# Performance work log

Hardware: AMD Instinct MI355X
Metric: run time of the kernel (lower is better)

## Reference

```python
import jax, jax.numpy as jnp
import numpy as np

CH = 192; NH = 8; HD = CH // NH; WS = 8; OV = 2; WSO = WS + 2 * OV
SCALE = HD ** -0.5
B, H, W = 2, 256, 256

# static relative-position index (matches WindowMSA._idx)
_gy, _gx = np.meshgrid(np.arange(WS), np.arange(WS), indexing='ij')
_flat = np.stack([_gy.ravel(), _gx.ravel()])            # [2, ws*ws]
_rel = _flat[:, :, None] - _flat[:, None, :]
_rel[0] += WS - 1; _rel[1] += WS - 1; _rel[0] *= 2 * WS - 1
RPE_IDX = jnp.asarray(_rel.sum(0), dtype=jnp.int32)     # [64, 64]


def _ln(x, g, b, eps=1e-5):
    m = jnp.mean(x, -1, keepdims=True)
    v = jnp.mean((x - m) ** 2, -1, keepdims=True)
    return (x - m) * jax.lax.rsqrt(v + eps) * g + b


def _partition(xhw):  # [B,H,W,C] -> [B*nw, ws*ws, C]
    b, h, w, c = xhw.shape
    x = xhw.reshape(b, h // WS, WS, w // WS, WS, c).transpose(0, 1, 3, 2, 4, 5)
    return x.reshape(-1, WS * WS, c)


def _reverse(xw, h, w, b):  # [B*nw, ws*ws, C] -> [B,H,W,C]
    c = xw.shape[-1]
    x = xw.reshape(b, h // WS, w // WS, WS, WS, c).transpose(0, 1, 3, 2, 4, 5)
    return x.reshape(b, h, w, c)


def _mha(q, k, v, bias=None):  # q:[n,Nq,C] k,v:[n,Nk,C] split into heads
    n, nq, c = q.shape
    nk = k.shape[1]
    q = q.reshape(n, nq, NH, HD).transpose(0, 2, 1, 3)
    k = k.reshape(n, nk, NH, HD).transpose(0, 2, 1, 3)
    v = v.reshape(n, nk, NH, HD).transpose(0, 2, 1, 3)
    attn = jnp.einsum('bhnd,bhmd->bhnm', q, k) * SCALE
    if bias is not None:
        attn = attn + bias
    attn = jax.nn.softmax(attn, axis=-1)
    out = jnp.einsum('bhnm,bhmd->bhnd', attn, v)
    return out.transpose(0, 2, 1, 3).reshape(n, nq, c)


def _forward(x, g1, b1, qkv_w, rpe, wproj_w, g2, b2, mlp_w1, mlp_w2,
             alpha, og, ob, q_w, kv_w, oproj_w):
    b, c, h, w = x.shape  # H,W are multiples of WS -> no window padding
    xhw = x.transpose(0, 2, 3, 1)  # BHWC

    # --- window MSA branch (shift=False) ---
    xw = _partition(xhw)  # [b*nw, 64, C]
    xn = _ln(xw, g1, b1)
    qkv = xn @ qkv_w.T  # [n, 64, 3C]
    q, k, v = jnp.split(qkv, 3, axis=-1)
    bias = rpe[RPE_IDX].transpose(2, 0, 1)[None]  # [1, nh, 64, 64]
    msa = _mha(q, k, v, bias) @ wproj_w.T
    xw = xw + msa
    hmid = _ln(xw, g2, b2) @ mlp_w1.T
    xw = xw + jax.nn.gelu(hmid, approximate=False) @ mlp_w2.T
    x_win = _reverse(xw, h, w, b).transpose(0, 3, 1, 2)  # BCHW

    # --- overlapping cross attention branch ---
    xwin = _partition(xhw)  # queries from non-overlapped windows [n, 64, C]
    q = _ln(xwin, og, ob) @ q_w.T
    xp2 = jnp.pad(x, ((0, 0), (0, 0), (OV, OV), (OV, OV)), mode='reflect')
    xp2 = xp2.transpose(0, 2, 3, 1)  # [B, H+2ov, W+2ov, C]
    nh_w, nw_w = h // WS, w // WS
    rows = (jnp.arange(nh_w) * WS)[:, None] + jnp.arange(WSO)[None, :]
    cols = (jnp.arange(nw_w) * WS)[:, None] + jnp.arange(WSO)[None, :]
    xuf = xp2[:, rows]            # [B, nh_w, wso, W+2ov, C]
    xuf = xuf[:, :, :, cols]      # [B, nh_w, wso, nw_w, wso, C]
    xuf = xuf.transpose(0, 1, 3, 2, 4, 5).reshape(-1, WSO * WSO, c)
    kv = xuf @ kv_w.T             # [n, 144, 2C]
    k, v = jnp.split(kv, 2, axis=-1)
    out = _mha(q, k, v) @ oproj_w.T + xwin
    x_oca = _reverse(out, h, w, b).transpose(0, 3, 1, 2)

    return x + x_win * alpha + x_oca * (1.0 - alpha)


def setup_inputs():
    key = jax.random.key(0)
    ks = jax.random.split(key, 10)
    f = lambda k, shape: jax.random.normal(k, shape, jnp.float32) * 0.02
    return {
        'x': jax.random.normal(ks[0], (B, CH, H, W), jnp.float32),
        'g1': jnp.ones((CH,), jnp.float32), 'b1': jnp.zeros((CH,), jnp.float32),
        'qkv_w': f(ks[1], (3 * CH, CH)),
        'rpe': f(ks[2], ((2 * WS - 1) ** 2, NH)),
        'wproj_w': f(ks[3], (CH, CH)),
        'g2': jnp.ones((CH,), jnp.float32), 'b2': jnp.zeros((CH,), jnp.float32),
        'mlp_w1': f(ks[4], (2 * CH, CH)), 'mlp_w2': f(ks[5], (CH, 2 * CH)),
        'alpha': jnp.float32(0.5),
        'og': jnp.ones((CH,), jnp.float32), 'ob': jnp.zeros((CH,), jnp.float32),
        'q_w': f(ks[6], (CH, CH)), 'kv_w': f(ks[7], (2 * CH, CH)),
        'oproj_w': f(ks[8], (CH, CH)),
    }


def reference(x, g1, b1, qkv_w, rpe, wproj_w, g2, b2, mlp_w1, mlp_w2,
              alpha, og, ob, q_w, kv_w, oproj_w):
    return _forward(x, g1, b1, qkv_w, rpe, wproj_w, g2, b2, mlp_w1, mlp_w2,
                    alpha, og, ob, q_w, kv_w, oproj_w)
```

## Files before the change

kernel.cpp:

```cpp
#include <hip/hip_runtime.h>
#include <hip/hip_bf16.h>

typedef unsigned short u16;
typedef unsigned int   u32;
typedef __attribute__((ext_vector_type(8))) short bf16x8;
typedef __attribute__((ext_vector_type(4))) float f32x4;

#define CH   192
#define NH   8
#define HWD  256
#define LDW  200
#define QSTR 28
#define SCALE 0.20412414523193154f

__device__ __forceinline__ float bf2f(u16 u){ u32 v = ((u32)u) << 16; return __builtin_bit_cast(float, v); }
__device__ __forceinline__ u16 f2bf(float f){
  u32 u = __builtin_bit_cast(u32, f);
  u = (u + 0x7fffu + ((u >> 16) & 1u)) >> 16;
  return (u16)u;
}
__device__ __forceinline__ float lo2f(u32 p){ return __builtin_bit_cast(float, p << 16); }
__device__ __forceinline__ float hi2f(u32 p){ return __builtin_bit_cast(float, p & 0xffff0000u); }
__device__ __forceinline__ void up8(uint4 q, float* f){
  f[0]=lo2f(q.x); f[1]=hi2f(q.x); f[2]=lo2f(q.y); f[3]=hi2f(q.y);
// ... 311 lines not shown
      for (int j = 0; j < 6; ++j)
        acc[j] = mfma16(a, bfrag(WO, (half*6 + j)*6 + kt, l), acc[j]);
    }
    __syncthreads();
    #pragma unroll
    for (int j = 0; j < 6; ++j){
      int col = (half*6 + j)*16 + (l & 15);
      #pragma unroll
      for (int r = 0; r < 4; ++r)
        pool[XO_ + (rbase + r)*LDW + col] = f2bf(acc[j][r]);
    }
  }
  __syncthreads();

  if (MODE == 0){
    float beta = 1.f - alpha_p[0];
    float xg = 1.f + beta;
    for (int j = tid; j < 1536; j += 512){
      int c = j >> 3, ty = j & 7;
      size_t goff = ((size_t)c*HWD + hrow + ty)*HWD + wcol;
      const float* src = xb + goff;
      float4 a = *reinterpret_cast<const float4*>(src);
      float4 q = *reinterpret_cast<const float4*>(src + 4);
      float wv[8];
      #pragma unroll
      for (int e = 0; e < 8; ++e) wv[e] = bf2f(pool[XO_ + (ty*8 + e)*LDW + c]);
      float4 o1 = make_float4(xg*a.x + beta*wv[0], xg*a.y + beta*wv[1], xg*a.z + beta*wv[2], xg*a.w + beta*wv[3]);
      float4 o2 = make_float4(xg*q.x + beta*wv[4], xg*q.y + beta*wv[5], xg*q.z + beta*wv[6], xg*q.w + beta*wv[7]);
      *reinterpret_cast<float4*>(outb + goff)     = o1;
      *reinterpret_cast<float4*>(outb + goff + 4) = o2;
    }
  } else {
    u16* xw = xoca + (size_t)win*12288;
    for (int j = tid; j < 1536; j += 512){
      int c = j >> 3, ty = j & 7;
      size_t goff = ((size_t)c*HWD + hrow + ty)*HWD + wcol;
      const float* src = xb + goff;
      float4 a = *reinterpret_cast<const float4*>(src);
      float4 q = *reinterpret_cast<const float4*>(src + 4);
      float xv[8] = {a.x,a.y,a.z,a.w,q.x,q.y,q.z,q.w};
      u32 wds[4];
      #pragma unroll
      for (int e = 0; e < 4; ++e){
        u32 lo = f2bf(bf2f(pool[XO_ + (ty*8 + 2*e  )*LDW + c]) + xv[2*e]);
        u32 hi = f2bf(bf2f(pool[XO_ + (ty*8 + 2*e+1)*LDW + c]) + xv[2*e+1]);
        wds[e] = lo | (hi << 16);
      }
      uint4 o; o.x = wds[0]; o.y = wds[1]; o.z = wds[2]; o.w = wds[3];
      *reinterpret_cast<uint4*>(xw + c*64 + ty*8) = o;
    }
  }
}

#define MSX  0
#define MSQ  12800
#define MKF  25600
#define MVT  41984
#define MP0  60416
#define MP1  65024
#define MSN  25600
#define MXW  38400
#define MSG  0
#define MSTM 69632
#define MSTS 70656
#define MST  71168
#define MPOOL 71424

template<int MODE>
__global__ __launch_bounds__(512) void k_msa(
    const float* __restrict__ x, const u16* __restrict__ ws16, const float* __restrict__ wsf,
    const float* __restrict__ rpe, const float* __restrict__ alpha_p, float* __restrict__ out,
    const u16* __restrict__ xoca)
{
  __shared__ __align__(16) u16 pool[MPOOL];
  float* stm = reinterpret_cast<float*>(pool + MSTM);
  float* sts = reinterpret_cast<float*>(pool + MSTS);
  float* st  = reinterpret_cast<float*>(pool + MST);
  const u16* W1  = ws16 + WS_W1/2;
  const u16* WP  = ws16 + WS_WP/2;
  const u16* WM1 = ws16 + WS_WM1/2;
  const u16* WM2 = ws16 + WS_WM2/2;
  const float* c1  = wsf + WS_C1/4;
  const float* c2  = wsf + WS_C2/4;
  const float* c1m = wsf + WS_C1M/4;
  const float* c2m = wsf + WS_C2M/4;

  const int tid = threadIdx.x;
  const int win = blockIdx.x;
  const int b  = win >> 10;
  const int wy = (win >> 5) & 31;
  const int wx = win & 31;
  const int hrow = wy*8, wcol = wx*8;
  const float* xb = x + (size_t)b*CH*HWD*HWD;
  float* outb = out + (size_t)b*CH*HWD*HWD;
  const f32x4 z4 = {0.f,0.f,0.f,0.f};

  for (int j = tid; j < 1536; j += 512){
    int c = j >> 3, ty = j & 7;
    const float* src = xb + ((size_t)c*HWD + hrow + ty)*HWD + wcol;
    float4 a = *reinterpret_cast<const float4*>(src);
    float4 q = *reinterpret_cast<const float4*>(src + 4);
    u16* dst = &pool[MSX + (ty*8)*LDW + c];
    dst[0*LDW]=f2bf(a.x); dst[1*LDW]=f2bf(a.y); dst[2*LDW]=f2bf(a.z); dst[3*LDW]=f2bf(a.w);
    dst[4*LDW]=f2bf(q.x); dst[5*LDW]=f2bf(q.y); dst[6*LDW]=f2bf(q.z); dst[7*LDW]=f2bf(q.w);
  }
  {
    const uint4 zz = make_uint4(0,0,0,0);
    for (int i = tid; i < 2048; i += 512)
      *reinterpret_cast<uint4*>(pool + MKF + i*8) = zz;
    for (int i = tid; i < 2304; i += 512)
      *reinterpret_cast<uint4*>(pool + MVT + i*8) = zz;
    for (int i = tid; i < 64; i += 512)
      *reinterpret_cast<uint4*>(pool + MSQ + i*LDW + 192) = zz;
  }
  __syncthreads();
  ln_stats(pool + MSX, st, tid);
  __syncthreads();

  const int w = tid >> 6, l = tid & 63;
  const int mt = w >> 1, half = w & 1;
  const int arow = mt*16 + (l & 15);
  const int rbase = mt*16 + ((l>>4)<<2);

  {
    f32x4 acc[18];
    #pragma unroll
    for (int j = 0; j < 18; ++j) acc[j] = z4;
    for (int kt = 0; kt < 6; ++kt){
      bf16x8 a = afrag(pool, MSX, LDW, arow, kt, l);
      #pragma unroll
      for (int j = 0; j < 18; ++j)
        acc[j] = mfma16(a, bfrag(W1, (half*18 + j)*6 + kt, l), acc[j]);
    }
    float mr[4], rr[4];
    #pragma unroll
    for (int r = 0; r < 4; ++r){ mr[r] = st[(rbase+r)*2]; rr[r] = st[(rbase+r)*2+1]; }
    #pragma unroll
    for (int j = 0; j < 18; ++j){
      int tile = half*18 + j;
      int col = tile*16 + (l & 15);
      float c1v = c1[col], c2v = c2[col];
      if (tile < 12){
        #pragma unroll
        for (int r = 0; r < 4; ++r){
          int row = rbase + r;
          float v = rr[r]*(acc[j][r] - mr[r]*c1v) + c2v;
          pool[MSQ + row*LDW + col] = f2bf(SCALE*v);
        }
      } else if (tile < 24){
        int d = col - 192; int h = d/24; int dd = d - h*24;
        int base = MKF + h*2048 + ((((dd>>3)<<4))<<3) + (dd&7);
        #pragma unroll
        for (int r = 0; r < 4; ++r){
          int row = rbase + r;
          float v = rr[r]*(acc[j][r] - mr[r]*c1v) + c2v;
          pool[base + ((row>>4)<<9) + ((row&15)<<3)] = f2bf(v);
        }
      } else {
        int d = col - 384; int h = d/24; int dd = d - h*24;
        int base = MVT + h*2304 + dd*72;
        #pragma unroll
        for (int r = 0; r < 4; ++r){
          int row = rbase + r;
          float v = rr[r]*(acc[j][r] - mr[r]*c1v) + c2v;
          pool[base + row] = f2bf(v);
        }
      }
    }
  }
  __syncthreads();

  {
    const int ng = half;
    int bidx[2][4];
    #pragma unroll
    for (int t = 0; t < 2; ++t)
      #pragma unroll
      for (int r = 0; r < 4; ++r){
        int row = rbase + r, col = (ng*2 + t)*16 + (l & 15);
        bidx[t][r] = (((row>>3)-(col>>3)+7)*15 + ((row&7)-(col&7)+7))*NH;
      }
    for (int hg = 0; hg < 2; ++hg){
      f32x4 S[4][2];
      #pragma unroll
      for (int hh = 0; hh < 4; ++hh){
        int h = hg*4 + hh;
        bf16x8 a = *reinterpret_cast<const bf16x8*>(pool + MSQ + arow*LDW + h*24 + ((l>>4)<<3));
        #pragma unroll
        for (int t = 0; t < 2; ++t)
          S[hh][t] = mfma16(a, *reinterpret_cast<const bf16x8*>(pool + MKF + h*2048 + (ng*2+t)*512 + l*8), z4);
      }
      #pragma unroll
      for (int hh = 0; hh < 4; ++hh){
        int h = hg*4 + hh;
        #pragma unroll
        for (int t = 0; t < 2; ++t)
          #pragma unroll
          for (int r = 0; r < 4; ++r)
            S[hh][t][r] += rpe[bidx[t][r] + h];
        #pragma unroll
        for (int r = 0; r < 4; ++r){
          float mx = fmaxf(S[hh][0][r], S[hh][1][r]);
          mx = fmaxf(mx, __shfl_xor(mx, 1, 64));
          mx = fmaxf(mx, __shfl_xor(mx, 2, 64));
          mx = fmaxf(mx, __shfl_xor(mx, 4, 64));
          mx = fmaxf(mx, __shfl_xor(mx, 8, 64));
          if ((l & 15) == 0) stm[hh*128 + (rbase+r)*2 + ng] = mx;
        }
      }
      __syncthreads();
      #pragma unroll
      for (int hh = 0; hh < 4; ++hh){
        int h = hg*4 + hh;
        u16* Pb = pool + ((h & 1) ? MP1 : MP0);
        float* sb = sts + (h & 1)*128;
        #pragma unroll
        for (int r = 0; r < 4; ++r){
          int row = rbase + r;
          float m = fmaxf(stm[hh*128 + row*2], stm[hh*128 + row*2 + 1]);
          float sum = 0.f;
          #pragma unroll
          for (int t = 0; t < 2; ++t){
            float p = __expf(S[hh][t][r] - m);
            sum += p;
            Pb[row*72 + (ng*2+t)*16 + (l & 15)] = f2bf(p);
          }
          sum += __shfl_xor(sum, 1, 64);
          sum += __shfl_xor(sum, 2, 64);
          sum += __shfl_xor(sum, 4, 64);
          sum += __shfl_xor(sum, 8, 64);
          if ((l & 15) == 0) sb[row*2 + ng] = sum;
        }
        __syncthreads();
        f32x4 O = z4;
        #pragma unroll
        for (int kt = 0; kt < 2; ++kt){
          bf16x8 pa = *reinterpret_cast<const bf16x8*>(Pb + arow*72 + kt*32 + ((l>>4)<<3));
          bf16x8 vb = *reinterpret_cast<const bf16x8*>(pool + MVT + h*2304 + (ng*16 + (l & 15))*72 + kt*32 + ((l>>4)<<3));
          O = mfma16(pa, vb, O);
        }
        int d = ng*16 + (l & 15);
        if (d < 24){
          #pragma unroll
          for (int r = 0; r < 4; ++r){
            int row = rbase + r;
            float inv = 1.f / (sb[row*2] + sb[row*2 + 1]);
            pool[MSQ + row*LDW + h*24 + d] = f2bf(O[r]*inv);
          }
        }
      }
    }
  }
  __syncthreads();

  {
    f32x4 acc[6];
    #pragma unroll
    for (int j = 0; j < 6; ++j) acc[j] = z4;
    for (int kt = 0; kt < 6; ++kt){
      bf16x8 a = afrag(pool, MSQ, LDW, arow, kt, l);
      #pragma unroll
      for (int j = 0; j < 6; ++j)
        acc[j] = mfma16(a, bfrag(WP, (half*6 + j)*6 + kt, l), acc[j]);
    }
    __syncthreads();
    #pragma unroll
    for (int j = 0; j < 6; ++j){
      int col = (half*6 + j)*16 + (l & 15);
      #pragma unroll
      for (int r = 0; r < 4; ++r){
        int row = rbase + r;
        pool[MSN + row*LDW + col] = f2bf(acc[j][r] + bf2f(pool[MSX + row*LDW + col]));
      }
    }
  }
  __syncthreads();
  ln_stats(pool + MSN, st, tid);
  __syncthreads();

  {
    f32x4 acc[12];
    #pragma unroll
    for (int j = 0; j < 12; ++j) acc[j] = z4;
    for (int kt = 0; kt < 6; ++kt){
      bf16x8 a = afrag(pool, MSN, LDW, arow, kt, l);
      #pragma unroll
      for (int j = 0; j < 12; ++j)
        acc[j] = mfma16(a, bfrag(WM1, (half*12 + j)*6 + kt, l), acc[j]);
    }
    float mr[4], rr[4];
    #pragma unroll
    for (int r = 0; r < 4; ++r){ mr[r] = st[(rbase+r)*2]; rr[r] = st[(rbase+r)*2+1]; }
    __syncthreads();
    #pragma unroll
    for (int j = 0; j < 12; ++j){
      int col = (half*12 + j)*16 + (l & 15);
      float c1v = c1m[col], c2v = c2m[col];
      #pragma unroll
      for (int r = 0; r < 4; ++r){
        float hv = rr[r]*(acc[j][r] - mr[r]*c1v) + c2v;
        float gl = 0.5f*hv*(1.f + erff(hv*0.70710678118654752f));
        pool[MSG + (rbase + r)*392 + col] = f2bf(gl);
      }
    }
  }
  __syncthreads();

  {
    f32x4 acc[6];
    #pragma unroll
    for (int j = 0; j < 6; ++j) acc[j] = z4;
    for (int kt = 0; kt < 12; ++kt){
      bf16x8 a = afrag(pool, MSG, 392, arow, kt, l);
      #pragma unroll
      for (int j = 0; j < 6; ++j)
        acc[j] = mfma16(a, bfrag(WM2, (half*6 + j)*12 + kt, l), acc[j]);
    }
    #pragma unroll
    for (int j = 0; j < 6; ++j){
      int col = (half*6 + j)*16 + (l & 15);
      #pragma unroll
      for (int r = 0; r < 4; ++r){
        int row = rbase + r;
        pool[MXW + row*LDW + col] = f2bf(acc[j][r] + bf2f(pool[MSN + row*LDW + col]));
      }
    }
  }
  __syncthreads();

  float alpha = alpha_p[0];
  if (MODE == 0){
    for (int j = tid; j < 1536; j += 512){
      int c = j >> 3, ty = j & 7;
      size_t goff = ((size_t)c*HWD + hrow + ty)*HWD + wcol;
      float* dst = outb + goff;
      float4 a = *reinterpret_cast<const float4*>(dst);
      float4 q = *reinterpret_cast<const float4*>(dst + 4);
      float wv[8];
      #pragma unroll
      for (int e = 0; e < 8; ++e) wv[e] = bf2f(pool[MXW + (ty*8 + e)*LDW + c]);
      float4 o1 = make_float4(a.x + alpha*wv[0], a.y + alpha*wv[1], a.z + alpha*wv[2], a.w + alpha*wv[3]);
      float4 o2 = make_float4(q.x + alpha*wv[4], q.y + alpha*wv[5], q.z + alpha*wv[6], q.w + alpha*wv[7]);
      *reinterpret_cast<float4*>(dst)     = o1;
      *reinterpret_cast<float4*>(dst + 4) = o2;
    }
  } else {
    float beta = 1.f - alpha;
    const u16* xw = xoca + (size_t)win*12288;
    for (int j = tid; j < 1536; j += 512){
      int c = j >> 3, ty = j & 7;
      size_t goff = ((size_t)c*HWD + hrow + ty)*HWD + wcol;
      const float* src = xb + goff;
      float4 a = *reinterpret_cast<const float4*>(src);
      float4 q = *reinterpret_cast<const float4*>(src + 4);
      uint4 oc = *reinterpret_cast<const uint4*>(xw + c*64 + ty*8);
      float ov[8]; up8(oc, ov);
      float wv[8];
      #pragma unroll
      for (int e = 0; e < 8; ++e) wv[e] = bf2f(pool[MXW + (ty*8 + e)*LDW + c]);
      float4 o1 = make_float4(a.x + alpha*wv[0] + beta*ov[0], a.y + alpha*wv[1] + beta*ov[1],
                              a.z + alpha*wv[2] + beta*ov[2], a.w + alpha*wv[3] + beta*ov[3]);
      float4 o2 = make_float4(q.x + alpha*wv[4] + beta*ov[4], q.y + alpha*wv[5] + beta*ov[5],
                              q.z + alpha*wv[6] + beta*ov[6], q.w + alpha*wv[7] + beta*ov[7]);
      *reinterpret_cast<float4*>(outb + goff)     = o1;
      *reinterpret_cast<float4*>(outb + goff + 4) = o2;
    }
  }
}

__device__ __forceinline__ void layernorm_fb(const u16* __restrict__ src, u16* __restrict__ dst,
                                             const float* __restrict__ g, const float* __restrict__ b,
                                             int tid)
{
  int r = tid >> 3, sub = tid & 7;
  const u16* row = src + r*LDW + sub*24;
  float v[24];
  float s = 0.f, s2 = 0.f;
  #pragma unroll
  for (int e = 0; e < 24; ++e){ v[e] = bf2f(row[e]); s += v[e]; s2 += v[e]*v[e]; }
  s  += __shfl_xor(s, 1, 64);  s  += __shfl_xor(s, 2, 64);  s  += __shfl_xor(s, 4, 64);
  s2 += __shfl_xor(s2, 1, 64); s2 += __shfl_xor(s2, 2, 64); s2 += __shfl_xor(s2, 4, 64);
  float m   = s * (1.f/192.f);
  float var = s2 * (1.f/192.f) - m*m;
  float rs  = rsqrtf(var + 1e-5f);
  u16* drow = dst + r*LDW + sub*24;
  #pragma unroll
  for (int e = 0; e < 24; ++e)
    drow[e] = f2bf((v[e] - m) * rs * g[sub*24+e] + b[sub*24+e]);
}
__device__ __forceinline__ void gemm83(const u16* __restrict__ a_lds,
                                       const float* __restrict__ w0,
                                       const float* __restrict__ w1,
                                       const float* __restrict__ w2,
                                       int tg, float (*acc)[3])
{
  for (int k0 = 0; k0 < 192; k0 += 8){
    float wv[3][8];
    ldw8(w0 + k0, wv[0]); ldw8(w1 + k0, wv[1]); ldw8(w2 + k0, wv[2]);
    #pragma unroll
    for (int tt = 0; tt < 8; ++tt){
      float a[8];
      up8(*reinterpret_cast<const uint4*>(a_lds + (tg*8+tt)*LDW + k0), a);
      #pragma unroll
      for (int e = 0; e < 8; ++e){
        acc[tt][0] += a[e]*wv[0][e];
        acc[tt][1] += a[e]*wv[1][e];
        acc[tt][2] += a[e]*wv[2][e];
      }
    }
  }
}
__global__ __launch_bounds__(512) void k_msa_fb(
// ... 368 lines not shown
```

Baseline: 950.6 us.

## Shrink MSA kernel LDS footprint by staging K/V per head-group

Shared memory for the window MSA kernel is cut from about 140KB to about 75KB. The QKV accumulators now stay in registers, and K/V are scattered into LDS four heads at a time, once per head group. The projection residual is re-read from global x instead of being kept in LDS, and a single P buffer replaces the double-buffered one. The goal is to fit two 512-thread blocks per CU for better latency hiding, at the cost of holding 18 accumulators in registers across the attention loop, extra barriers, and uncoalesced global reads for the residual.

Measured after the change: 1.191 ms, median of 4. 1.25x slower.

```diff
diff --git a/kernel.cpp b/kernel.cpp
--- a/kernel.cpp
+++ b/kernel.cpp
@@ -387,19 +387,18 @@
   }
 }
 
-#define MSX  0
-#define MSQ  12800
-#define MKF  25600
-#define MVT  41984
-#define MP0  60416
-#define MP1  65024
-#define MSN  25600
-#define MXW  38400
-#define MSG  0
-#define MSTM 69632
-#define MSTS 70656
-#define MST  71168
-#define MPOOL 71424
+#define KFGm  0
+#define VTGm  8192
+#define MSXm  0
+#define MSQm  17408
+#define PBUFm 30208
+#define STMm  34816
+#define STSm  35840
+#define MSNm  0
+#define MSGm  12800
+#define MXWm  12800
+#define STLNm 37888
+#define MPOOLm 38144
 
 template<int MODE>
 __global__ __launch_bounds__(512) void k_msa(
@@ -407,10 +406,10 @@
     const float* __restrict__ rpe, const float* __restrict__ alpha_p, float* __restrict__ out,
     const u16* __restrict__ xoca)
 {
-  __shared__ __align__(16) u16 pool[MPOOL];
-  float* stm = reinterpret_cast<float*>(pool + MSTM);
-  float* sts = reinterpret_cast<float*>(pool + MSTS);
-  float* st  = reinterpret_cast<float*>(pool + MST);
+  __shared__ __align__(16) u16 pool[MPOOLm];
+  float* stm = reinterpret_cast<float*>(pool + STMm);
+  float* sts = reinterpret_cast<float*>(pool + STSm);
+  float* st  = reinterpret_cast<float*>(pool + STLNm);
   const u16* W1  = ws16 + WS_W1/2;
   const u16* WP  = ws16 + WS_WP/2;
   const u16* WM1 = ws16 + WS_WM1/2;
@@ -435,229 +434,249 @@
     const float* src = xb + ((size_t)c*HWD + hrow + ty)*HWD + wcol;
     float4 a = *reinterpret_cast<const float4*>(src);
     float4 q = *reinterpret_cast<const float4*>(src + 4);
-    u16* dst = &pool[MSX + (ty*8)*LDW + c];
+    u16* dst = &pool[MSXm + (ty*8)*LDW + c];
     dst[0*LDW]=f2bf(a.x); dst[1*LDW]=f2bf(a.y); dst[2*LDW]=f2bf(a.z); dst[3*LDW]=f2bf(a.w);
     dst[4*LDW]=f2bf(q.x); dst[5*LDW]=f2bf(q.y); dst[6*LDW]=f2bf(q.z); dst[7*LDW]=f2bf(q.w);
   }
   {
     const uint4 zz = make_uint4(0,0,0,0);
-    for (int i = tid; i < 2048; i += 512)
-      *reinterpret_cast<uint4*>(pool + MKF + i*8) = zz;
-    for (int i = tid; i < 2304; i += 512)
-      *reinterpret_cast<uint4*>(pool + MVT + i*8) = zz;
     for (int i = tid; i < 64; i += 512)
-      *reinterpret_cast<uint4*>(pool + MSQ + i*LDW + 192) = zz;
-  }
-  __syncthreads();
-  ln_stats(pool + MSX, st, tid);
+      *reinterpret_cast<uint4*>(pool + MSQm + i*LDW + 192) = zz;
+  }
+  __syncthreads();
+  ln_stats(pool + MSXm, st, tid);
   __syncthreads();
 
   const int w = tid >> 6, l = tid & 63;
   const int mt = w >> 1, half = w & 1;
   const int arow = mt*16 + (l & 15);
   const int rbase = mt*16 + ((l>>4)<<2);
+  const int ng = half;
+
+  f32x4 acc[18];
+  #pragma unroll
+  for (int j = 0; j < 18; ++j) acc[j] = z4;
+  for (int kt = 0; kt < 6; ++kt){
+    bf16x8 a = afrag(pool, MSXm, LDW, arow, kt, l);
+    #pragma unroll
+    for (int j = 0; j < 18; ++j)
+      acc[j] = mfma16(a, bfrag(W1, (half*18 + j)*6 + kt, l), acc[j]);
+  }
+  float mr[4], rr[4];
+  #pragma unroll
+  for (int r = 0; r < 4; ++r){ mr[r] = st[(rbase+r)*2]; rr[r] = st[(rbase+r)*2+1]; }
+  __syncthreads();
+
+  #define SCAT(J, TILE) do{                                                     \
+    int col = (TILE)*16 + (l & 15);                                             \
+    float c1v = c1[col], c2v = c2[col];                                         \
+    if ((TILE) < 12){                                                           \
+      _Pragma("unroll")                                                         \
+      for (int r = 0; r < 4; ++r){                                              \
+        int row = rbase + r;                                                    \
+        float v = rr[r]*(acc[J][r] - mr[r]*c1v) + c2v;                          \
+        pool[MSQm + row*LDW + col] = f2bf(SCALE*v);                             \
+      }                                                                         \
+    } else if ((TILE) < 24){                                                    \
+      int d = col - 192; int h = d/24; int dd = d - h*24;                       \
+      int base = KFGm + (h&3)*2048 + ((dd>>3)<<7) + (dd&7);                     \
+      _Pragma("unroll")                                                         \
+      for (int r = 0; r < 4; ++r){                                              \
+        int row = rbase + r;                                                    \
+        float v = rr[r]*(acc[J][r] - mr[r]*c1v) + c2v;                          \
+        pool[base + ((row>>4)<<9) + ((row&15)<<3)] = f2bf(v);                   \
+      }                                                                         \
+    } else {                                                                    \
+      int d = col - 384; int h = d/24; int dd = d - h*24;                       \
+      int base = VTGm + (h&3)*2304 + dd*72;                                     \
+      _Pragma("unroll")                                                         \
+      for (int r = 0; r < 4; ++r){                                              \
+        int row = rbase + r;                                                    \
+        float v = rr[r]*(acc[J][r] - mr[r]*c1v) + c2v;                          \
+        pool[base + row] = f2bf(v);                                             \
+      }                                                                         \
+    }                                                                           \
+  } while(0)
 
   {
-    f32x4 acc[18];
-    #pragma unroll
-    for (int j = 0; j < 18; ++j) acc[j] = z4;
-    for (int kt = 0; kt < 6; ++kt){
-      bf16x8 a = afrag(pool, MSX, LDW, arow, kt, l);
-      #pragma unroll
-      for (int j = 0; j < 18; ++j)
-        acc[j] = mfma16(a, bfrag(W1, (half*18 + j)*6 + kt, l), acc[j]);
-    }
-    float mr[4], rr[4];
-    #pragma unroll
-    for (int r = 0; r < 4; ++r){ mr[r] = st[(rbase+r)*2]; rr[r] = st[(rbase+r)*2+1]; }
-    #pragma unroll
-    for (int j = 0; j < 18; ++j){
-      int tile = half*18 + j;
-      int col = tile*16 + (l & 15);
-      float c1v = c1[col], c2v = c2[col];
-      if (tile < 12){
+    const uint4 zz = make_uint4(0,0,0,0);
+    for (int i = tid; i < 256; i += 512)
+      *reinterpret_cast<uint4*>(pool + KFGm + (i>>4)*512 + (48 + (i&15))*8) = zz;
+    for (int i = tid; i < 288; i += 512){
+      int slot = i/72; int t2 = i - slot*72; int dd = 24 + t2/9; int seg = t2 - (t2/9)*9;
+      *reinterpret_cast<uint4*>(pool + VTGm + slot*2304 + dd*72 + seg*8) = zz;
+    }
+  }
+
+  int bidx[2][4];
+  #pragma unroll
+  for (int t = 0; t < 2; ++t)
+    #pragma unroll
+    for (int r = 0; r < 4; ++r){
+      int row = rbase + r, col = (ng*2 + t)*16 + (l & 15);
+      bidx[t][r] = (((row>>3)-(col>>3)+7)*15 + ((row&7)-(col&7)+7))*NH;
+    }
+
+  for (int hg = 0; hg < 2; ++hg){
+    if (hg == 0){
+      if (half == 0){
+        #pragma unroll
+        for (int j = 0; j < 18; ++j) SCAT(j, j);
+      } else {
+        #pragma unroll
+        for (int j = 6; j < 12; ++j) SCAT(j, 18 + j);
+      }
+    } else {
+      if (half == 1){
+        #pragma unroll
+        for (int j = 0; j < 6; ++j)  SCAT(j, 18 + j);
+        #pragma unroll
+        for (int j = 12; j < 18; ++j) SCAT(j, 18 + j);
+      }
+    }
+    __syncthreads();
+
+    f32x4 S[4][2];
+    #pragma unroll
+    for (int hh = 0; hh < 4; ++hh){
+      int h = hg*4 + hh;
+      bf16x8 a = *reinterpret_cast<const bf16x8*>(pool + MSQm + arow*LDW + h*24 + ((l>>4)<<3));
+      #pragma unroll
+      for (int t = 0; t < 2; ++t)
+        S[hh][t] = mfma16(a, *reinterpret_cast<const bf16x8*>(pool + KFGm + (h&3)*2048 + (ng*2+t)*512 + l*8), z4);
+    }
+    #pragma unroll
+    for (int hh = 0; hh < 4; ++hh){
+      int h = hg*4 + hh;
+      #pragma unroll
+      for (int t = 0; t < 2; ++t)
+        #pragma unroll
+        for (int r = 0; r < 4; ++r)
+          S[hh][t][r] += rpe[bidx[t][r] + h];
+      #pragma unroll
+      for (int r = 0; r < 4; ++r){
+        float mx = fmaxf(S[hh][0][r], S[hh][1][r]);
+        mx = fmaxf(mx, __shfl_xor(mx, 1, 64));
+        mx = fmaxf(mx, __shfl_xor(mx, 2, 64));
+        mx = fmaxf(mx, __shfl_xor(mx, 4, 64));
+        mx = fmaxf(mx, __shfl_xor(mx, 8, 64));
+        if ((l & 15) == 0) stm[hh*128 + (rbase+r)*2 + ng] = mx;
+      }
+    }
+    __syncthreads();
+
+    #pragma unroll
+    for (int hh = 0; hh < 4; ++hh){
+      int h = hg*4 + hh;
+      #pragma unroll
+      for (int r = 0; r < 4; ++r){
+        int row = rbase + r;
+        float m = fmaxf(stm[hh*128 + row*2], stm[hh*128 + row*2 + 1]);
+        float sum = 0.f;
+        #pragma unroll
+        for (int t = 0; t < 2; ++t){
+          float p = __expf(S[hh][t][r] - m);
+          sum += p;
+          pool[PBUFm + row*72 + (ng*2+t)*16 + (l & 15)] = f2bf(p);
+        }
+        sum += __shfl_xor(sum, 1, 64);
+        sum += __shfl_xor(sum, 2, 64);
+        sum += __shfl_xor(sum, 4, 64);
+        sum += __shfl_xor(sum, 8, 64);
+        if ((l & 15) == 0) sts[row*2 + ng] = sum;
+      }
+      __syncthreads();
+      f32x4 O = z4;
+      #pragma unroll
+      for (int kt = 0; kt < 2; ++kt){
+        bf16x8 pa = *reinterpret_cast<const bf16x8*>(pool + PBUFm + arow*72 + kt*32 + ((l>>4)<<3));
+        bf16x8 vb = *reinterpret_cast<const bf16x8*>(pool + VTGm + (h&3)*2304 + (ng*16 + (l & 15))*72 + kt*32 + ((l>>4)<<3));
+        O = mfma16(pa, vb, O);
+      }
+      int d = ng*16 + (l & 15);
+      if (d < 24){
         #pragma unroll
         for (int r = 0; r < 4; ++r){
           int row = rbase + r;
-          float v = rr[r]*(acc[j][r] - mr[r]*c1v) + c2v;
-          pool[MSQ + row*LDW + col] = f2bf(SCALE*v);
+          float inv = 1.f / (sts[row*2] + sts[row*2 + 1]);
+          pool[MSQm + row*LDW + h*24 + d] = f2bf(O[r]*inv);
         }
-      } else if (tile < 24){
-        int d = col - 192; int h = d/24; int dd = d - h*24;
-        int base = MKF + h*2048 + ((((dd>>3)<<4))<<3) + (dd&7);
-        #pragma unroll
-        for (int r = 0; r < 4; ++r){
-          int row = rbase + r;
-          float v = rr[r]*(acc[j][r] - mr[r]*c1v) + c2v;
-          pool[base + ((row>>4)<<9) + ((row&15)<<3)] = f2bf(v);
-        }
-      } else {
-        int d = col - 384; int h = d/24; int dd = d - h*24;
-        int base = MVT + h*2304 + dd*72;
-        #pragma unroll
-        for (int r = 0; r < 4; ++r){
-          int row = rbase + r;
-          float v = rr[r]*(acc[j][r] - mr[r]*c1v) + c2v;
-          pool[base + row] = f2bf(v);
-        }
-      }
-    }
-  }
-  __syncthreads();
+      }
+      __syncthreads();
+    }
+  }
+  #undef SCAT
 
   {
-    const int ng = half;
-    int bidx[2][4];
-    #pragma unroll
-    for (int t = 0; t < 2; ++t)
-      #pragma unroll
-      for (int r = 0; r < 4; ++r){
-        int row = rbase + r, col = (ng*2 + t)*16 + (l & 15);
-        bidx[t][r] = (((row>>3)-(col>>3)+7)*15 + ((row&7)-(col&7)+7))*NH;
-      }
-    for (int hg = 0; hg < 2; ++hg){
-      f32x4 S[4][2];
-      #pragma unroll
-      for (int hh = 0; hh < 4; ++hh){
-        int h = hg*4 + hh;
-        bf16x8 a = *reinterpret_cast<const bf16x8*>(pool + MSQ + arow*LDW + h*24 + ((l>>4)<<3));
-        #pragma unroll
-        for (int t = 0; t < 2; ++t)
-          S[hh][t] = mfma16(a, *reinterpret_cast<const bf16x8*>(pool + MKF + h*2048 + (ng*2+t)*512 + l*8), z4);
-      }
-      #pragma unroll
-      for (int hh = 0; hh < 4; ++hh){
-        int h = hg*4 + hh;
-        #pragma unroll
-        for (int t = 0; t < 2; ++t)
-          #pragma unroll
-          for (int r = 0; r < 4; ++r)
-            S[hh][t][r] += rpe[bidx[t][r] + h];
-        #pragma unroll
-        for (int r = 0; r < 4; ++r){
-          float mx = fmaxf(S[hh][0][r], S[hh][1][r]);
-          mx = fmaxf(mx, __shfl_xor(mx, 1, 64));
-          mx = fmaxf(mx, __shfl_xor(mx, 2, 64));
-          mx = fmaxf(mx, __shfl_xor(mx, 4, 64));
-          mx = fmaxf(mx, __shfl_xor(mx, 8, 64));
-          if ((l & 15) == 0) stm[hh*128 + (rbase+r)*2 + ng] = mx;
-        }
-      }
-      __syncthreads();
-      #pragma unroll
-      for (int hh = 0; hh < 4; ++hh){
-        int h = hg*4 + hh;
-        u16* Pb = pool + ((h & 1) ? MP1 : MP0);
-        float* sb = sts + (h & 1)*128;
-        #pragma unroll
-        for (int r = 0; r < 4; ++r){
-          int row = rbase + r;
-          float m = fmaxf(stm[hh*128 + row*2], stm[hh*128 + row*2 + 1]);
-          float sum = 0.f;
-          #pragma unroll
-          for (int t = 0; t < 2; ++t){
-            float p = __expf(S[hh][t][r] - m);
-            sum += p;
-            Pb[row*72 + (ng*2+t)*16 + (l & 15)] = f2bf(p);
-          }
-          sum += __shfl_xor(sum, 1, 64);
-          sum += __shfl_xor(sum, 2, 64);
-          sum += __shfl_xor(sum, 4, 64);
-          sum += __shfl_xor(sum, 8, 64);
-          if ((l & 15) == 0) sb[row*2 + ng] = sum;
-        }
-        __syncthreads();
-        f32x4 O = z4;
-        #pragma unroll
-        for (int kt = 0; kt < 2; ++kt){
-          bf16x8 pa = *reinterpret_cast<const bf16x8*>(Pb + arow*72 + kt*32 + ((l>>4)<<3));
-          bf16x8 vb = *reinterpret_cast<const bf16x8*>(pool + MVT + h*2304 + (ng*16 + (l & 15))*72 + kt*32 + ((l>>4)<<3));
-          O = mfma16(pa, vb, O);
-        }
-        int d = ng*16 + (l & 15);
-        if (d < 24){
-          #pragma unroll
-          for (int r = 0; r < 4; ++r){
-            int row = rbase + r;
-            float inv = 1.f / (sb[row*2] + sb[row*2 + 1]);
-            pool[MSQ + row*LDW + h*24 + d] = f2bf(O[r]*inv);
-          }
-        }
-      }
-    }
-  }
-  __syncthreads();
-
-  {
-    f32x4 acc[6];
-    #pragma unroll
-    for (int j = 0; j < 6; ++j) acc[j] = z4;
+    f32x4 acc3[6];
+    #pragma unroll
+    for (int j = 0; j < 6; ++j) acc3[j] = z4;
     for (int kt = 0; kt < 6; ++kt){
-      bf16x8 a = afrag(pool, MSQ, LDW, arow, kt, l);
+      bf16x8 a = afrag(pool, MSQm, LDW, arow, kt, l);
       #pragma unroll
       for (int j = 0; j < 6; ++j)
-        acc[j] = mfma16(a, bfrag(WP, (half*6 + j)*6 + kt, l), acc[j]);
-    }
-    __syncthreads();
+        acc3[j] = mfma16(a, bfrag(WP, (half*6 + j)*6 + kt, l), acc3[j]);
+    }
     #pragma unroll
     for (int j = 0; j < 6; ++j){
       int col = (half*6 + j)*16 + (l & 15);
       #pragma unroll
       for (int r = 0; r < 4; ++r){
         int row = rbase + r;
-        pool[MSN + row*LDW + col] = f2bf(acc[j][r] + bf2f(pool[MSX + row*LDW + col]));
-      }
-    }
-  }
-  __syncthreads();
-  ln_stats(pool + MSN, st, tid);
+        float xres = xb[(size_t)col*65536 + (size_t)(hrow + (row>>3))*HWD + wcol + (row&7)];
+        pool[MSNm + row*LDW + col] = f2bf(acc3[j][r] + xres);
+      }
+    }
+  }
+  __syncthreads();
+  ln_stats(pool + MSNm, st, tid);
   __syncthreads();
 
   {
-    f32x4 acc[12];
-    #pragma unroll
-    for (int j = 0; j < 12; ++j) acc[j] = z4;
+    f32x4 acc5[12];
+    #pragma unroll
+    for (int j = 0; j < 12; ++j) acc5[j] = z4;
     for (int kt = 0; kt < 6; ++kt){
-      bf16x8 a = afrag(pool, MSN, LDW, arow, kt, l);
+      bf16x8 a = afrag(pool, MSNm, LDW, arow, kt, l);
       #pragma unroll
       for (int j = 0; j < 12; ++j)
-        acc[j] = mfma16(a, bfrag(WM1, (half*12 + j)*6 + kt, l), acc[j]);
-    }
-    float mr[4], rr[4];
-    #pragma unroll
-    for (int r = 0; r < 4; ++r){ mr[r] = st[(rbase+r)*2]; rr[r] = st[(rbase+r)*2+1]; }
-    __syncthreads();
+        acc5[j] = mfma16(a, bfrag(WM1, (half*12 + j)*6 + kt, l), acc5[j]);
+    }
+    float m2[4], r2[4];
+    #pragma unroll
+    for (int r = 0; r < 4; ++r){ m2[r] = st[(rbase+r)*2]; r2[r] = st[(rbase+r)*2+1]; }
     #pragma unroll
     for (int j = 0; j < 12; ++j){
       int col = (half*12 + j)*16 + (l & 15);
       float c1v = c1m[col], c2v = c2m[col];
       #pragma unroll
       for (int r = 0; r < 4; ++r){
-        float hv = rr[r]*(acc[j][r] - mr[r]*c1v) + c2v;
+        float hv = r2[r]*(acc5[j][r] - m2[r]*c1v) + c2v;
         float gl = 0.5f*hv*(1.f + erff(hv*0.70710678118654752f));
-        pool[MSG + (rbase + r)*392 + col] = f2bf(gl);
+        pool[MSGm + (rbase + r)*392 + col] = f2bf(gl);
       }
     }
   }
   __syncthreads();
 
   {
-    f32x4 acc[6];
-    #pragma unroll
-    for (int j = 0; j < 6; ++j) acc[j] = z4;
+    f32x4 acc6[6];
+    #pragma unroll
+    for (int j = 0; j < 6; ++j) acc6[j] = z4;
     for (int kt = 0; kt < 12; ++kt){
-      bf16x8 a = afrag(pool, MSG, 392, arow, kt, l);
+      bf16x8 a = afrag(pool, MSGm, 392, arow, kt, l);
       #pragma unroll
       for (int j = 0; j < 6; ++j)
-        acc[j] = mfma16(a, bfrag(WM2, (half*6 + j)*12 + kt, l), acc[j]);
-    }
+        acc6[j] = mfma16(a, bfrag(WM2, (half*6 + j)*12 + kt, l), acc6[j]);
+    }
+    __syncthreads();
     #pragma unroll
     for (int j = 0; j < 6; ++j){
       int col = (half*6 + j)*16 + (l & 15);
       #pragma unroll
       for (int r = 0; r < 4; ++r){
         int row = rbase + r;
-        pool[MXW + row*LDW + col] = f2bf(acc[j][r] + bf2f(pool[MSN + row*LDW + col]));
+        pool[MXWm + row*LDW + col] = f2bf(acc6[j][r] + bf2f(pool[MSNm + row*LDW + col]));
       }
     }
   }
@@ -673,7 +692,7 @@
       float4 q = *reinterpret_cast<const float4*>(dst + 4);
       float wv[8];
       #pragma unroll
-      for (int e = 0; e < 8; ++e) wv[e] = bf2f(pool[MXW + (ty*8 + e)*LDW + c]);
+      for (int e = 0; e < 8; ++e) wv[e] = bf2f(pool[MXWm + (ty*8 + e)*LDW + c]);
       float4 o1 = make_float4(a.x + alpha*wv[0], a.y + alpha*wv[1], a.z + alpha*wv[2], a.w + alpha*wv[3]);
       float4 o2 = make_float4(q.x + alpha*wv[4], q.y + alpha*wv[5], q.z + alpha*wv[6], q.w + alpha*wv[7]);
       *reinterpret_cast<float4*>(dst)     = o1;
@@ -692,7 +711,7 @@
       float ov[8]; up8(oc, ov);
       float wv[8];
       #pragma unroll
-      for (int e = 0; e < 8; ++e) wv[e] = bf2f(pool[MXW + (ty*8 + e)*LDW + c]);
+      for (int e = 0; e < 8; ++e) wv[e] = bf2f(pool[MXWm + (ty*8 + e)*LDW + c]);
       float4 o1 = make_float4(a.x + alpha*wv[0] + beta*ov[0], a.y + alpha*wv[1] + beta*ov[1],
                               a.z + alpha*wv[2] + beta*ov[2], a.w + alpha*wv[3] + beta*ov[3]);
       float4 o2 = make_float4(q.x + alpha*wv[4] + beta*ov[4], q.y + alpha*wv[5] + beta*ov[5],
```

## Interleave QKV projection with per-head-pair attention to shrink LDS footprint

Applied to the files above, without the earlier changes.

The window MSA kernel now computes K and V tiles for two heads at a time, interleaved with the attention for those heads, instead of materialising all of Q, K and V in shared memory up front. Buffers are reused aggressively: the residual overwrites the input tile, and the GELU and output buffers alias the Q region. This cuts the LDS pool from about 143KB to about 79KB, likely allowing two 512-thread blocks per CU, and reduces accumulator registers. The cost is more __syncthreads barriers per head pair and repeated A-fragment loads across the four projection passes.

Measured after the change: 1.025 ms. 1.08x slower.

```diff
diff --git a/kernel.cpp b/kernel.cpp
--- a/kernel.cpp
+++ b/kernel.cpp
@@ -387,19 +387,17 @@
   }
 }
 
-#define MSX  0
-#define MSQ  12800
-#define MKF  25600
-#define MVT  41984
-#define MP0  60416
-#define MP1  65024
-#define MSN  25600
-#define MXW  38400
-#define MSG  0
-#define MSTM 69632
-#define MSTS 70656
-#define MST  71168
-#define MPOOL 71424
+#define XB_   0
+#define MQ_   12800
+#define KFG_  25600
+#define VTG_  29696
+#define PB_   34304
+#define GEL_  12800
+#define XWN_  12800
+#define STM3  38912
+#define STS3  39168
+#define STL3  39424
+#define MPOOL3 39680
 
 template<int MODE>
 __global__ __launch_bounds__(512) void k_msa(
@@ -407,10 +405,10 @@
     const float* __restrict__ rpe, const float* __restrict__ alpha_p, float* __restrict__ out,
     const u16* __restrict__ xoca)
 {
-  __shared__ __align__(16) u16 pool[MPOOL];
-  float* stm = reinterpret_cast<float*>(pool + MSTM);
-  float* sts = reinterpret_cast<float*>(pool + MSTS);
-  float* st  = reinterpret_cast<float*>(pool + MST);
+  __shared__ __align__(16) u16 pool[MPOOL3];
+  float* stm = reinterpret_cast<float*>(pool + STM3);
+  float* sts = reinterpret_cast<float*>(pool + STS3);
+  float* st  = reinterpret_cast<float*>(pool + STL3);
   const u16* W1  = ws16 + WS_W1/2;
   const u16* WP  = ws16 + WS_WP/2;
   const u16* WM1 = ws16 + WS_WM1/2;
@@ -435,70 +433,151 @@
     const float* src = xb + ((size_t)c*HWD + hrow + ty)*HWD + wcol;
     float4 a = *reinterpret_cast<const float4*>(src);
     float4 q = *reinterpret_cast<const float4*>(src + 4);
-    u16* dst = &pool[MSX + (ty*8)*LDW + c];
+    u16* dst = &pool[XB_ + (ty*8)*LDW + c];
     dst[0*LDW]=f2bf(a.x); dst[1*LDW]=f2bf(a.y); dst[2*LDW]=f2bf(a.z); dst[3*LDW]=f2bf(a.w);
     dst[4*LDW]=f2bf(q.x); dst[5*LDW]=f2bf(q.y); dst[6*LDW]=f2bf(q.z); dst[7*LDW]=f2bf(q.w);
   }
   {
     const uint4 zz = make_uint4(0,0,0,0);
-    for (int i = tid; i < 2048; i += 512)
-      *reinterpret_cast<uint4*>(pool + MKF + i*8) = zz;
-    for (int i = tid; i < 2304; i += 512)
-      *reinterpret_cast<uint4*>(pool + MVT + i*8) = zz;
     for (int i = tid; i < 64; i += 512)
-      *reinterpret_cast<uint4*>(pool + MSQ + i*LDW + 192) = zz;
-  }
-  __syncthreads();
-  ln_stats(pool + MSX, st, tid);
+      *reinterpret_cast<uint4*>(pool + MQ_ + i*LDW + 192) = zz;
+    for (int i = tid; i < 128; i += 512)
+      *reinterpret_cast<uint4*>(pool + KFG_ + (i>>4)*512 + 384 + (i&15)*8) = zz;
+    for (int i = tid; i < 144; i += 512){
+      int slot = i/72, t2 = i - slot*72;
+      int dd = 24 + t2/9, seg = t2 - (t2/9)*9;
+      *reinterpret_cast<uint4*>(pool + VTG_ + slot*2304 + dd*72 + seg*8) = zz;
+    }
+  }
+  __syncthreads();
+  ln_stats(pool + XB_, st, tid);
   __syncthreads();
 
   const int w = tid >> 6, l = tid & 63;
-  const int mt = w >> 1, half = w & 1;
+  const int mt = w >> 1, half = w & 1, ng = half;
   const int arow = mt*16 + (l & 15);
   const int rbase = mt*16 + ((l>>4)<<2);
 
-  {
-    f32x4 acc[18];
-    #pragma unroll
-    for (int j = 0; j < 18; ++j) acc[j] = z4;
+  float mr[4], rr[4];
+  #pragma unroll
+  for (int r = 0; r < 4; ++r){ mr[r] = st[(rbase+r)*2]; rr[r] = st[(rbase+r)*2+1]; }
+
+  int bidx[2][4];
+  #pragma unroll
+  for (int t = 0; t < 2; ++t)
+    #pragma unroll
+    for (int r = 0; r < 4; ++r){
+      int row = rbase + r, col = (ng*2 + t)*16 + (l & 15);
+      bidx[t][r] = (((row>>3)-(col>>3)+7)*15 + ((row&7)-(col&7)+7))*NH;
+    }
+
+  for (int hg = 0; hg < 4; ++hg){
+    const int tK0 = half ? (13+3*hg) : (12+3*hg);
+    const int tK1 = half ? (24+3*hg) : (14+3*hg);
+    const int tK2 = half ? (26+3*hg) : (25+3*hg);
+    f32x4 acc[9];
+    #pragma unroll
+    for (int j = 0; j < 9; ++j) acc[j] = z4;
     for (int kt = 0; kt < 6; ++kt){
-      bf16x8 a = afrag(pool, MSX, LDW, arow, kt, l);
-      #pragma unroll
-      for (int j = 0; j < 18; ++j)
-        acc[j] = mfma16(a, bfrag(W1, (half*18 + j)*6 + kt, l), acc[j]);
-    }
-    float mr[4], rr[4];
-    #pragma unroll
-    for (int r = 0; r < 4; ++r){ mr[r] = st[(rbase+r)*2]; rr[r] = st[(rbase+r)*2+1]; }
-    #pragma unroll
-    for (int j = 0; j < 18; ++j){
-      int tile = half*18 + j;
+      bf16x8 a = afrag(pool, XB_, LDW, arow, kt, l);
+      if (hg == 0){
+        #pragma unroll
+        for (int j = 0; j < 6; ++j)
+          acc[j] = mfma16(a, bfrag(W1, (2*j+half)*6 + kt, l), acc[j]);
+      }
+      acc[6] = mfma16(a, bfrag(W1, tK0*6 + kt, l), acc[6]);
+      acc[7] = mfma16(a, bfrag(W1, tK1*6 + kt, l), acc[7]);
+      acc[8] = mfma16(a, bfrag(W1, tK2*6 + kt, l), acc[8]);
+    }
+    __syncthreads();
+    if (hg == 0){
+      #pragma unroll
+      for (int j = 0; j < 6; ++j){
+        int col = (2*j+half)*16 + (l & 15);
+        float c1v = c1[col], c2v = c2[col];
+        #pragma unroll
+        for (int r = 0; r < 4; ++r){
+          int row = rbase + r;
+          pool[MQ_ + row*LDW + col] = f2bf(SCALE*(rr[r]*(acc[j][r] - mr[r]*c1v) + c2v));
+        }
+      }
+    }
+    #pragma unroll
+    for (int j = 0; j < 3; ++j){
+      int tile = (j == 0) ? tK0 : (j == 1) ? tK1 : tK2;
       int col = tile*16 + (l & 15);
       float c1v = c1[col], c2v = c2[col];
-      if (tile < 12){
+      if (tile < 24){
+        int d = col - 192; int h = d/24; int dd = d - h*24; int slot = h & 1;
         #pragma unroll
         for (int r = 0; r < 4; ++r){
           int row = rbase + r;
-          float v = rr[r]*(acc[j][r] - mr[r]*c1v) + c2v;
-          pool[MSQ + row*LDW + col] = f2bf(SCALE*v);
+          float v = rr[r]*(acc[6+j][r] - mr[r]*c1v) + c2v;
+          pool[KFG_ + slot*2048 + ((row>>4)<<9) + ((dd>>3)<<7) + ((row&15)<<3) + (dd&7)] = f2bf(v);
         }
-      } else if (tile < 24){
-        int d = col - 192; int h = d/24; int dd = d - h*24;
-        int base = MKF + h*2048 + ((((dd>>3)<<4))<<3) + (dd&7);
+      } else {
+        int d = col - 384; int h = d/24; int dd = d - h*24; int slot = h & 1;
         #pragma unroll
         for (int r = 0; r < 4; ++r){
           int row = rbase + r;
-          float v = rr[r]*(acc[j][r] - mr[r]*c1v) + c2v;
-          pool[base + ((row>>4)<<9) + ((row&15)<<3)] = f2bf(v);
+          float v = rr[r]*(acc[6+j][r] - mr[r]*c1v) + c2v;
+          pool[VTG_ + slot*2304 + dd*72 + row] = f2bf(v);
         }
-      } else {
-        int d = col - 384; int h = d/24; int dd = d - h*24;
-        int base = MVT + h*2304 + dd*72;
+      }
+    }
+    __syncthreads();
+
+    #pragma unroll
+    for (int hh = 0; hh < 2; ++hh){
+      int h = hg*2 + hh;
+      f32x4 S0, S1;
+      {
+        bf16x8 a = *reinterpret_cast<const bf16x8*>(pool + MQ_ + arow*LDW + h*24 + ((l>>4)<<3));
+        S0 = mfma16(a, *reinterpret_cast<const bf16x8*>(pool + KFG_ + hh*2048 + (ng*2+0)*512 + l*8), z4);
+        S1 = mfma16(a, *reinterpret_cast<const bf16x8*>(pool + KFG_ + hh*2048 + (ng*2+1)*512 + l*8), z4);
+      }
+      #pragma unroll
+      for (int r = 0; r < 4; ++r){ S0[r] += rpe[bidx[0][r] + h]; S1[r] += rpe[bidx[1][r] + h]; }
+      #pragma unroll
+      for (int r = 0; r < 4; ++r){
+        float mx = fmaxf(S0[r], S1[r]);
+        mx = fmaxf(mx, __shfl_xor(mx, 1, 64));
+        mx = fmaxf(mx, __shfl_xor(mx, 2, 64));
+        mx = fmaxf(mx, __shfl_xor(mx, 4, 64));
+        mx = fmaxf(mx, __shfl_xor(mx, 8, 64));
+        if ((l & 15) == 0) stm[(rbase+r)*2 + ng] = mx;
+      }
+      __syncthreads();
+      #pragma unroll
+      for (int r = 0; r < 4; ++r){
+        int row = rbase + r;
+        float m = fmaxf(stm[row*2], stm[row*2 + 1]);
+        float p0 = __expf(S0[r] - m);
+        float p1 = __expf(S1[r] - m);
+        pool[PB_ + row*72 + (ng*2+0)*16 + (l & 15)] = f2bf(p0);
+        pool[PB_ + row*72 + (ng*2+1)*16 + (l & 15)] = f2bf(p1);
+        float sum = p0 + p1;
+        sum += __shfl_xor(sum, 1, 64);
+        sum += __shfl_xor(sum, 2, 64);
+        sum += __shfl_xor(sum, 4, 64);
+        sum += __shfl_xor(sum, 8, 64);
+        if ((l & 15) == 0) sts[row*2 + ng] = sum;
+      }
+      __syncthreads();
+      f32x4 O = z4;
+      #pragma unroll
+      for (int kt = 0; kt < 2; ++kt){
+        bf16x8 pa = *reinterpret_cast<const bf16x8*>(pool + PB_ + arow*72 + kt*32 + ((l>>4)<<3));
+        bf16x8 vb = *reinterpret_cast<const bf16x8*>(pool + VTG_ + hh*2304 + (ng*16 + (l & 15))*72 + kt*32 + ((l>>4)<<3));
+        O = mfma16(pa, vb, O);
+      }
+      int d = ng*16 + (l & 15);
+      if (d < 24){
         #pragma unroll
         for (int r = 0; r < 4; ++r){
           int row = rbase + r;
-          float v = rr[r]*(acc[j][r] - mr[r]*c1v) + c2v;
-          pool[base + row] = f2bf(v);
+          float inv = 1.f / (sts[row*2] + sts[row*2 + 1]);
+          pool[MQ_ + row*LDW + h*24 + d] = f2bf(O[r]*inv);
         }
       }
     }
@@ -506,158 +585,75 @@
   __syncthreads();
 
   {
-    const int ng = half;
-    int bidx[2][4];
-    #pragma unroll
-    for (int t = 0; t < 2; ++t)
-      #pragma unroll
-      for (int r = 0; r < 4; ++r){
-        int row = rbase + r, col = (ng*2 + t)*16 + (l & 15);
-        bidx[t][r] = (((row>>3)-(col>>3)+7)*15 + ((row&7)-(col&7)+7))*NH;
-      }
-    for (int hg = 0; hg < 2; ++hg){
-      f32x4 S[4][2];
-      #pragma unroll
-      for (int hh = 0; hh < 4; ++hh){
-        int h = hg*4 + hh;
-        bf16x8 a = *reinterpret_cast<const bf16x8*>(pool + MSQ + arow*LDW + h*24 + ((l>>4)<<3));
-        #pragma unroll
-        for (int t = 0; t < 2; ++t)
-          S[hh][t] = mfma16(a, *reinterpret_cast<const bf16x8*>(pool + MKF + h*2048 + (ng*2+t)*512 + l*8), z4);
-      }
-      #pragma unroll
-      for (int hh = 0; hh < 4; ++hh){
-        int h = hg*4 + hh;
-        #pragma unroll
-        for (int t = 0; t < 2; ++t)
-          #pragma unroll
-          for (int r = 0; r < 4; ++r)
-            S[hh][t][r] += rpe[bidx[t][r] + h];
-        #pragma unroll
-        for (int r = 0; r < 4; ++r){
-          float mx = fmaxf(S[hh][0][r], S[hh][1][r]);
-          mx = fmaxf(mx, __shfl_xor(mx, 1, 64));
-          mx = fmaxf(mx, __shfl_xor(mx, 2, 64));
-          mx = fmaxf(mx, __shfl_xor(mx, 4, 64));
-          mx = fmaxf(mx, __shfl_xor(mx, 8, 64));
-          if ((l & 15) == 0) stm[hh*128 + (rbase+r)*2 + ng] = mx;
-        }
-      }
-      __syncthreads();
-      #pragma unroll
-      for (int hh = 0; hh < 4; ++hh){
-        int h = hg*4 + hh;
-        u16* Pb = pool + ((h & 1) ? MP1 : MP0);
-        float* sb = sts + (h & 1)*128;
-        #pragma unroll
-        for (int r = 0; r < 4; ++r){
-          int row = rbase + r;
-          float m = fmaxf(stm[hh*128 + row*2], stm[hh*128 + row*2 + 1]);
-          float sum = 0.f;
-          #pragma unroll
-          for (int t = 0; t < 2; ++t){
-            float p = __expf(S[hh][t][r] - m);
-            sum += p;
-            Pb[row*72 + (ng*2+t)*16 + (l & 15)] = f2bf(p);
-          }
-          sum += __shfl_xor(sum, 1, 64);
-          sum += __shfl_xor(sum, 2, 64);
-          sum += __shfl_xor(sum, 4, 64);
-          sum += __shfl_xor(sum, 8, 64);
-          if ((l & 15) == 0) sb[row*2 + ng] = sum;
-        }
-        __syncthreads();
-        f32x4 O = z4;
-        #pragma unroll
-        for (int kt = 0; kt < 2; ++kt){
-          bf16x8 pa = *reinterpret_cast<const bf16x8*>(Pb + arow*72 + kt*32 + ((l>>4)<<3));
-          bf16x8 vb = *reinterpret_cast<const bf16x8*>(pool + MVT + h*2304 + (ng*16 + (l & 15))*72 + kt*32 + ((l>>4)<<3));
-          O = mfma16(pa, vb, O);
-        }
-        int d = ng*16 + (l & 15);
-        if (d < 24){
-          #pragma unroll
-          for (int r = 0; r < 4; ++r){
-            int row = rbase + r;
-            float inv = 1.f / (sb[row*2] + sb[row*2 + 1]);
-            pool[MSQ + row*LDW + h*24 + d] = f2bf(O[r]*inv);
-          }
-        }
-      }
-    }
-  }
-  __syncthreads();
-
-  {
-    f32x4 acc[6];
-    #pragma unroll
-    for (int j = 0; j < 6; ++j) acc[j] = z4;
+    f32x4 acc3[6];
+    #pragma unroll
+    for (int j = 0; j < 6; ++j) acc3[j] = z4;
     for (int kt = 0; kt < 6; ++kt){
-      bf16x8 a = afrag(pool, MSQ, LDW, arow, kt, l);
+      bf16x8 a = afrag(pool, MQ_, LDW, arow, kt, l);
       #pragma unroll
       for (int j = 0; j < 6; ++j)
-        acc[j] = mfma16(a, bfrag(WP, (half*6 + j)*6 + kt, l), acc[j]);
-    }
-    __syncthreads();
+        acc3[j] = mfma16(a, bfrag(WP, (half*6 + j)*6 + kt, l), acc3[j]);
+    }
     #pragma unroll
     for (int j = 0; j < 6; ++j){
       int col = (half*6 + j)*16 + (l & 15);
       #pragma unroll
       for (int r = 0; r < 4; ++r){
         int row = rbase + r;
-        pool[MSN + row*LDW + col] = f2bf(acc[j][r] + bf2f(pool[MSX + row*LDW + col]));
-      }
-    }
-  }
-  __syncthreads();
-  ln_stats(pool + MSN, st, tid);
+        float v = acc3[j][r] + bf2f(pool[XB_ + row*LDW + col]);
+        pool[XB_ + row*LDW + col] = f2bf(v);
+      }
+    }
+  }
+  __syncthreads();
+  ln_stats(pool + XB_, st, tid);
   __syncthreads();
 
   {
-    f32x4 acc[12];
-    #pragma unroll
-    for (int j = 0; j < 12; ++j) acc[j] = z4;
+    f32x4 acc5[12];
+    #pragma unroll
+    for (int j = 0; j < 12; ++j) acc5[j] = z4;
     for (int kt = 0; kt < 6; ++kt){
-      bf16x8 a = afrag(pool, MSN, LDW, arow, kt, l);
+      bf16x8 a = afrag(pool, XB_, LDW, arow, kt, l);
       #pragma unroll
       for (int j = 0; j < 12; ++j)
-        acc[j] = mfma16(a, bfrag(WM1, (half*12 + j)*6 + kt, l), acc[j]);
-    }
-    float mr[4], rr[4];
-    #pragma unroll
-    for (int r = 0; r < 4; ++r){ mr[r] = st[(rbase+r)*2]; rr[r] = st[(rbase+r)*2+1]; }
-    __syncthreads();
+        acc5[j] = mfma16(a, bfrag(WM1, (half*12 + j)*6 + kt, l), acc5[j]);
+    }
+    float m2[4], r2[4];
+    #pragma unroll
+    for (int r = 0; r < 4; ++r){ m2[r] = st[(rbase+r)*2]; r2[r] = st[(rbase+r)*2+1]; }
     #pragma unroll
     for (int j = 0; j < 12; ++j){
       int col = (half*12 + j)*16 + (l & 15);
       float c1v = c1m[col], c2v = c2m[col];
       #pragma unroll
       for (int r = 0; r < 4; ++r){
-        float hv = rr[r]*(acc[j][r] - mr[r]*c1v) + c2v;
+        float hv = r2[r]*(acc5[j][r] - m2[r]*c1v) + c2v;
         float gl = 0.5f*hv*(1.f + erff(hv*0.70710678118654752f));
-        pool[MSG + (rbase + r)*392 + col] = f2bf(gl);
+        pool[GEL_ + (rbase + r)*392 + col] = f2bf(gl);
       }
     }
   }
   __syncthreads();
 
   {
-    f32x4 acc[6];
-    #pragma unroll
-    for (int j = 0; j < 6; ++j) acc[j] = z4;
+    f32x4 acc6[6];
+    #pragma unroll
+    for (int j = 0; j < 6; ++j) acc6[j] = z4;
     for (int kt = 0; kt < 12; ++kt){
-      bf16x8 a = afrag(pool, MSG, 392, arow, kt, l);
+      bf16x8 a = afrag(pool, GEL_, 392, arow, kt, l);
       #pragma unroll
       for (int j = 0; j < 6; ++j)
-        acc[j] = mfma16(a, bfrag(WM2, (half*6 + j)*12 + kt, l), acc[j]);
-    }
+        acc6[j] = mfma16(a, bfrag(WM2, (half*6 + j)*12 + kt, l), acc6[j]);
+    }
+    __syncthreads();
     #pragma unroll
     for (int j = 0; j < 6; ++j){
       int col = (half*6 + j)*16 + (l & 15);
       #pragma unroll
       for (int r = 0; r < 4; ++r){
         int row = rbase + r;
-        pool[MXW + row*LDW + col] = f2bf(acc[j][r] + bf2f(pool[MSN + row*LDW + col]));
+        pool[XWN_ + row*LDW + col] = f2bf(acc6[j][r] + bf2f(pool[XB_ + row*LDW + col]));
       }
     }
   }
@@ -673,7 +669,7 @@
       float4 q = *reinterpret_cast<const float4*>(dst + 4);
       float wv[8];
       #pragma unroll
-      for (int e = 0; e < 8; ++e) wv[e] = bf2f(pool[MXW + (ty*8 + e)*LDW + c]);
+      for (int e = 0; e < 8; ++e) wv[e] = bf2f(pool[XWN_ + (ty*8 + e)*LDW + c]);
       float4 o1 = make_float4(a.x + alpha*wv[0], a.y + alpha*wv[1], a.z + alpha*wv[2], a.w + alpha*wv[3]);
       float4 o2 = make_float4(q.x + alpha*wv[4], q.y + alpha*wv[5], q.z + alpha*wv[6], q.w + alpha*wv[7]);
       *reinterpret_cast<float4*>(dst)     = o1;
@@ -692,7 +688,7 @@
       float ov[8]; up8(oc, ov);
       float wv[8];
       #pragma unroll
-      for (int e = 0; e < 8; ++e) wv[e] = bf2f(pool[MXW + (ty*8 + e)*LDW + c]);
+      for (int e = 0; e < 8; ++e) wv[e] = bf2f(pool[XWN_ + (ty*8 + e)*LDW + c]);
       float4 o1 = make_float4(a.x + alpha*wv[0] + beta*ov[0], a.y + alpha*wv[1] + beta*ov[1],
                               a.z + alpha*wv[2] + beta*ov[2], a.w + alpha*wv[3] + beta*ov[3]);
       float4 o2 = make_float4(q.x + alpha*wv[4] + beta*ov[4], q.y + alpha*wv[5] + beta*ov[5],
```
